# Kernel optimization log

Measured on AMD Instinct MI355X. Metric: run time of the kernel, lower is better.

## Reference

```python
import jax, jax.numpy as jnp
import numpy as np

B, N, F = 1024, 256, 8
E = 1024
OUT = 128          # NNConv out-channels (hardcoded in module)
N_DIV = 64         # len(num_actions)
PER = 3            # actions per diverter
FEAT = N * OUT     # feature_size() = num_nodes * 128


def setup_inputs() -> dict:
    key = jax.random.key(0)
    ks = jax.random.split(key, 20)
    s = lambda *sh: 0.02
    return {
        "x": jax.random.normal(ks[0], (B, N, F), jnp.float32),
        "edge_index": jax.random.randint(ks[1], (2, E), 0, N, jnp.int64),
        # edge-MLP nn1: Linear(1,64) -> ReLU -> Linear(64, F*OUT)
        "w1": jax.random.normal(ks[2], (1, 64), jnp.float32) * 0.1,
        "b1": jnp.zeros((64,), jnp.float32),
        "w2": jax.random.normal(ks[3], (64, F * OUT), jnp.float32) * 0.02,
        "b2": jnp.zeros((F * OUT,), jnp.float32),
        # NNConv root weight + bias
        "root_w": jax.random.normal(ks[4], (F, OUT), jnp.float32) * 0.1,
        "conv_b": jnp.zeros((OUT,), jnp.float32),
        # dueling heads
        "adv_w": jax.random.normal(ks[5], (FEAT, N_DIV * PER), jnp.float32) * 0.005,
        "adv_b": jnp.zeros((N_DIV * PER,), jnp.float32),
        "v1w": jax.random.normal(ks[6], (FEAT, 64), jnp.float32) * 0.005,
        "v1b": jnp.zeros((64,), jnp.float32),
        "v2w": jax.random.normal(ks[7], (64, 64), jnp.float32) * 0.1,
        "v2b": jnp.zeros((64,), jnp.float32),
        "v3w": jax.random.normal(ks[8], (64, N_DIV), jnp.float32) * 0.1,
        "v3b": jnp.zeros((N_DIV,), jnp.float32),
    }


def reference(x, edge_index, w1, b1, w2, b2, root_w, conv_b,
              adv_w, adv_b, v1w, v1b, v2w, v2b, v3w, v3b):
    b, n, f = x.shape
    out_c = root_w.shape[1]
    n_div = v3w.shape[1]
    flat = x.reshape(b * n, f)                              # [B*N, F]
    e = edge_index.shape[1]
    # edge_attr = ones -> edge MLP produces per-edge weight matrix theta
    ea = jnp.ones((e, 1), x.dtype)
    h = jax.nn.relu(ea @ w1 + b1)
    theta = (h @ w2 + b2).reshape(e, f, out_c)              # [E, F, OUT]
    src, tgt = edge_index[0], edge_index[1]
    # gather source feats -> per-edge matmul -> scatter-add at targets
    msg = jnp.einsum('ef,efo->eo', flat[src], theta)        # [E, OUT]
    agg = jnp.zeros((b * n, out_c), x.dtype).at[tgt].add(msg)
    conv = agg + flat @ root_w + conv_b                      # NNConv root + bias
    feat = jax.nn.relu(conv).reshape(b, -1)                  # [B, N*OUT]
    adv = jax.nn.relu(feat @ adv_w + adv_b).reshape(b, n_div, -1)
    val = jax.nn.relu(feat @ v1w + v1b)
    val = jax.nn.relu(val @ v2w + v2b)
    val = val @ v3w + v3b                                    # [B, n_div]
    return val[..., None] + adv - adv.mean(-1, keepdims=True)
```

## Files before the change

### kernel.cpp

```cpp
#include <hip/hip_runtime.h>

#define Bsz 1024
#define Nn 256
#define Fdim 8
#define Eedge 1024
#define OUTC 128
#define CADV 192
#define CTOT 256
#define Ktot 32768
#define ASTR 40
#define XSTR 24

typedef __attribute__((ext_vector_type(8))) short short8;
typedef __attribute__((ext_vector_type(4))) float float4v;

static __device__ inline unsigned short f2bf(float f) {
  union { float f; unsigned u; } v; v.f = f;
  unsigned r = v.u + 0x7FFFu + ((v.u >> 16) & 1u);
  return (unsigned short)(r >> 16);
}
static __device__ inline float bf2f(unsigned short h) {
  union { unsigned u; float f; } v; v.u = ((unsigned)h) << 16;
  return v.f;
}
static __device__ inline uint4 pack8(const unsigned short* b) {
  uint4 v;
  v.x = (unsigned)b[0] | ((unsigned)b[1] << 16);
  v.y = (unsigned)b[2] | ((unsigned)b[3] << 16);
  v.z = (unsigned)b[4] | ((unsigned)b[5] << 16);
  v.w = (unsigned)b[6] | ((unsigned)b[7] << 16);
  return v;
}
static __device__ inline unsigned cvtpk(float a, float b) {
  unsigned r;
  asm("v_cvt_pk_bf16_f32 %0, %1, %2" : "=v"(r) : "v"(a), "v"(b));
  return r;
}
static __device__ inline float hi_of(unsigned p)  {
  union { unsigned u; float f; } v; v.u = p << 16; return v.f;
}
static __device__ inline float hi2_of(unsigned p) {
  union { unsigned u; float f; } v; v.u = p & 0xFFFF0000u; return v.f;
}

__global__ __launch_bounds__(256) void prep_feat_kernel(
    const float* __restrict__ x, const int* __restrict__ ei,
    const float* __restrict__ w1, const float* __restrict__ b1,
    const float* __restrict__ w2, const float* __restrict__ b2,
    const float* __restrict__ rootw, const float* __restrict__ convb,
    const float* __restrict__ advw, const float* __restrict__ v1w,
    unsigned short* __restrict__ wt, unsigned short* __restrict__ feat0)
{
  __shared__ __align__(16) char smem[20480];
  int bid = blockIdx.x, t = threadIdx.x;

  if (bid < 16) {
    float* fs   = (float*)smem;
    float* h_s  = fs;
    float* rw_s = fs + 64;
    float* th_s = fs + 128;
    float* pt_s = fs + 192;
    float* S_s  = fs + 448;
    int*   flag = (int*)(fs + 2496);
    int obase = bid * 8;

    if (t < 64) {
      h_s[t]  = fmaxf(w1[t] + b1[t], 0.f);
      rw_s[t] = rootw[(t >> 3) * OUTC + obase + (t & 7)];
    }
    for (int i = t; i < Nn * Fdim; i += 256) S_s[i] = 0.f;
    if (t == 0) {
      int z = 0;
      for (int i = 1; i < 16; i += 2) z |= ei[i];
      *flag = (z == 0);
    }
    __syncthreads();
    int is64 = *flag;

    {
      int l = t & 63, g = t >> 6;
      int c = (l >> 3) * 128 + obase + (l & 7);
      float p = 0.f;
#pragma unroll
      for (int j = 0; j < 16; ++j)
        p += h_s[g * 16 + j] * w2[(size_t)(g * 16 + j) * 1024 + c];
      pt_s[t] = p;
    }
    int srcs[4], tgts[4];
#pragma unroll
    for (int q = 0; q < 4; ++q) {
      int e = t + q * 256;
      if (is64) { srcs[q] = ei[2 * e]; tgts[q] = ei[2 * (Eedge + e)]; }
      else      { srcs[q] = ei[e];     tgts[q] = ei[Eedge + e]; }
      srcs[q] &= 255; tgts[q] &= 255;
    }
    __syncthreads();
    if (t < 64) {
      int c = (t >> 3) * 128 + obase + (t & 7);
      th_s[t] = b2[c] + pt_s[t] + pt_s[t + 64] + pt_s[t + 128] + pt_s[t + 192];
    }
#pragma unroll
    for (int q = 0; q < 4; ++q) {
      const float* xp = x + srcs[q] * Fdim;
#pragma unroll
      for (int f = 0; f < Fdim; ++f)
        atomicAdd(&S_s[tgts[q] * Fdim + f], xp[f]);
    }
    __syncthreads();
    {
      int n = t;
      const float* xp = x + n * Fdim;
      float4 xa = *(const float4*)xp;
      float4 xb = *(const float4*)(xp + 4);
      float xv[8] = {xa.x, xa.y, xa.z, xa.w, xb.x, xb.y, xb.z, xb.w};
      float sv[8];
#pragma unroll
      for (int f = 0; f < 8; ++f) sv[f] = S_s[n * Fdim + f];
      unsigned short buf[8];
#pragma unroll
      for (int oi = 0; oi < 8; ++oi) {
        float z = convb[obase + oi];
#pragma unroll
        for (int f = 0; f < 8; ++f)
          z += xv[f] * rw_s[f * 8 + oi] + sv[f] * th_s[f * 8 + oi];
        buf[oi] = f2bf(fmaxf(z, 0.f));
      }
      *(uint4*)(feat0 + (size_t)n * OUTC + obase) = pack8(buf);
    }
  } else {
    unsigned short* st = (unsigned short*)smem;
    int kt = bid - 16, c = t;
    const float* src; int stride, col;
    if (c < CADV) { src = advw; stride = CADV; col = c; }
    else          { src = v1w;  stride = 64;   col = c - CADV; }
    float v[32];
#pragma unroll
    for (int i = 0; i < 32; ++i)
      v[i] = src[(size_t)(kt * 32 + i) * stride + col];
    unsigned pk[16];
#pragma unroll
    for (int i = 0; i < 16; ++i) pk[i] = cvtpk(v[2 * i], v[2 * i + 1]);
#pragma unroll
    for (int p = 0; p < 4; ++p) {
      uint4 w4; w4.x = pk[p * 4]; w4.y = pk[p * 4 + 1];
      w4.z = pk[p * 4 + 2]; w4.w = pk[p * 4 + 3];
      *(uint4*)(st + c * ASTR + p * 8) = w4;
    }
    __syncthreads();
    uint4* dst = (uint4*)(wt + (size_t)kt * (CTOT * 32));
    for (int r = 0; r < 4; ++r) {
      int s = r * 256 + c;
      dst[s] = *(const uint4*)(st + (s >> 2) * ASTR + (s & 3) * 8);
    }
  }
}

__global__ __launch_bounds__(512, 2) void gemm_mfma(
    const float* __restrict__ x, const unsigned short* __restrict__ wt,
    const float* __restrict__ rootw, const float* __restrict__ convb,
    const unsigned short* __restrict__ feat0, float* __restrict__ part,
    int iters, int ns)
{
  __shared__ short a_s[2][128 * ASTR];
  __shared__ short b_s[2][256 * ASTR];
  __shared__ short x_s[2][128 * XSTR];
  __shared__ short rw_s[128 * XSTR];
  __shared__ float convb_s[128];
  int t = threadIdx.x;
  int ch = blockIdx.x;
  int mb = blockIdx.y;
  int wave = t >> 6, lane = t & 63;
  int wm = wave >> 2, wn = wave & 3;
  int lm = lane & 15, lq = lane >> 4;

  float4v acc[4][4];
#pragma unroll
  for (int i = 0; i < 4; ++i)
#pragma unroll
    for (int j = 0; j < 4; ++j) acc[i][j] = (float4v)0.f;

  int kt0 = ch * iters;
  int iters4 = iters >> 2;
  int n0 = ch * iters4;
  int wr0 = (t >> 2) * ASTR + (t & 3) * 8;
  int u1 = t + 512;
  int wr1 = (u1 >> 2) * ASTR + (u1 & 3) * 8;

  if (t < 128) {
    float wv[8];
#pragma unroll
    for (int f = 0; f < 8; ++f) wv[f] = rootw[f * OUTC + t];
    unsigned ph[4];
#pragma unroll
    for (int i = 0; i < 4; ++i) ph[i] = cvtpk(wv[2 * i], wv[2 * i + 1]);
    float wl[8];
#pragma unroll
    for (int i = 0; i < 4; ++i) {
      wl[2 * i]     = wv[2 * i]     - hi_of(ph[i]);
      wl[2 * i + 1] = wv[2 * i + 1] - hi2_of(ph[i]);
    }
    unsigned pl[4];
#pragma unroll
    for (int i = 0; i < 4; ++i) pl[i] = cvtpk(wl[2 * i], wl[2 * i + 1]);
    uint4 wh4; wh4.x = ph[0]; wh4.y = ph[1]; wh4.z = ph[2]; wh4.w = ph[3];
    uint4 wl4; wl4.x = pl[0]; wl4.y = pl[1]; wl4.z = pl[2]; wl4.w = pl[3];
    *(uint4*)(rw_s + t * XSTR)     = wh4;
    *(uint4*)(rw_s + t * XSTR + 8) = wl4;
    convb_s[t] = convb[t];
  }
  int xr = (t & 255) >> 1, xh = t & 1;
  const float* xgb = x + ((size_t)(mb * 128 + xr) * Nn) * Fdim + xh * 4;
  if (t < 256) {
    float4 xv = *(const float4*)(xgb + (size_t)n0 * Fdim);
    uint2 dh, dl;
    dh.x = cvtpk(xv.x, xv.y);
    dh.y = cvtpk(xv.z, xv.w);
    dl.x = cvtpk(xv.x - hi_of(dh.x), xv.y - hi2_of(dh.x));
    dl.y = cvtpk(xv.z - hi_of(dh.y), xv.w - hi2_of(dh.y));
    *(uint2*)(x_s[0] + xr * XSTR + xh * 4)     = dh;
    *(uint2*)(x_s[0] + xr * XSTR + 8 + xh * 4) = dl;
  }
  __syncthreads();

  {
    int bloc = wave * 16 + lm;
    short8 xf = (short8)0;
    if (lq == 0 || lq == 2) xf = *(const short8*)(x_s[0] + bloc * XSTR);
    else if (lq == 1)       xf = *(const short8*)(x_s[0] + bloc * XSTR + 8);
#pragma unroll
    for (int tt = 0; tt < 2; ++tt) {
      int ot = tt;
      short8 wf = (short8)0;
      if (lq <= 1)      wf = *(const short8*)(rw_s + (ot * 16 + lm) * XSTR);
      else if (lq == 2) wf = *(const short8*)(rw_s + (ot * 16 + lm) * XSTR + 8);
      float4v c = __builtin_amdgcn_mfma_f32_16x16x32_bf16(wf, xf, (float4v)0.f, 0, 0, 0);
      int o0 = ot * 16 + lq * 4;
      float4 cb = *(const float4*)(convb_s + o0);
      unsigned d0 = cvtpk(fmaxf(c[0] + cb.x, 0.f), fmaxf(c[1] + cb.y, 0.f));
      unsigned d1 = cvtpk(fmaxf(c[2] + cb.z, 0.f), fmaxf(c[3] + cb.w, 0.f));
      if (mb == 0 && bloc == 0) {
        const unsigned* f0p = (const unsigned*)(feat0 + ((size_t)n0 * OUTC + o0));
        d0 = f0p[0]; d1 = f0p[1];
      }
      uint2 dd; dd.x = d0; dd.y = d1;
      *(uint2*)(a_s[0] + bloc * ASTR + tt * 16 + lq * 4) = dd;
    }
  }

  const uint4* gB = (const uint4*)wt + (size_t)kt0 * 1024;
  uint4 vb0 = gB[t], vb1 = gB[t + 512];
  float4 xpf = {0.f, 0.f, 0.f, 0.f};

  for (int kk = 0; kk < iters; ++kk) {
    int g = kk & 3, grp = kk >> 2;
    short* bb = b_s[kk & 1];
    *(uint4*)(bb + wr0) = vb0;
    *(uint4*)(bb + wr1) = vb1;
    if (g == 0 && grp + 1 < iters4 && t < 256)
      xpf = *(const float4*)(xgb + (size_t)(n0 + grp + 1) * Fdim);
    if (g == 3 && grp + 1 < iters4 && t < 256) {
      uint2 dh, dl;
      dh.x = cvtpk(xpf.x, xpf.y);
      dh.y = cvtpk(xpf.z, xpf.w);
      dl.x = cvtpk(xpf.x - hi_of(dh.x), xpf.y - hi2_of(dh.x));
      dl.y = cvtpk(xpf.z - hi_of(dh.y), xpf.w - hi2_of(dh.y));
      short* xd = x_s[(grp + 1) & 1];
      *(uint2*)(xd + xr * XSTR + xh * 4)     = dh;
      *(uint2*)(xd + xr * XSTR + 8 + xh * 4) = dl;
    }
    if (kk + 1 < iters) {
      const uint4* gB2 = (const uint4*)wt + (size_t)(kt0 + kk + 1) * 1024;
      vb0 = gB2[t]; vb1 = gB2[t + 512];
    }
    __syncthreads();

    short* ab = a_s[kk & 1];
    short8 aF[4];
#pragma unroll
    for (int i = 0; i < 4; ++i)
      aF[i] = *(const short8*)(ab + (wm * 64 + i * 16 + lm) * ASTR + lq * 8);
#pragma unroll
    for (int j = 0; j < 4; ++j) {
      short8 bF = *(const short8*)(bb + (wn * 64 + j * 16 + lm) * ASTR + lq * 8);
#pragma unroll
      for (int i = 0; i < 4; ++i)
        acc[i][j] = __builtin_amdgcn_mfma_f32_16x16x32_bf16(bF, aF[i], acc[i][j], 0, 0, 0);
    }

    if (kk + 1 < iters) {
      int kn = kk + 1;
      int g2 = kn & 3, grp2 = kn >> 2;
      const short* xs = x_s[grp2 & 1];
      int node2 = n0 + grp2;
      short* ad = a_s[kn & 1];
      int bloc = wave * 16 + lm;
      short8 xf = (short8)0;
      if (lq == 0 || lq == 2) xf = *(const short8*)(xs + bloc * XSTR);
      else if (lq == 1)       xf = *(const short8*)(xs + bloc * XSTR + 8);
#pragma unroll
      for (int tt = 0; tt < 2; ++tt) {
        int ot = g2 * 2 + tt;
        short8 wf = (short8)0;
        if (lq <= 1)      wf = *(const short8*)(rw_s + (ot * 16 + lm) * XSTR);
        else if (lq == 2) wf = *(const short8*)(rw_s + (ot * 16 + lm) * XSTR + 8);
        float4v c = __builtin_amdgcn_mfma_f32_16x16x32_bf16(wf, xf, (float4v)0.f, 0, 0, 0);
        int o0 = ot * 16 + lq * 4;
        float4 cb = *(const float4*)(convb_s + o0);
        unsigned d0 = cvtpk(fmaxf(c[0] + cb.x, 0.f), fmaxf(c[1] + cb.y, 0.f));
        unsigned d1 = cvtpk(fmaxf(c[2] + cb.z, 0.f), fmaxf(c[3] + cb.w, 0.f));
        if (mb == 0 && bloc == 0) {
          const unsigned* f0p = (const unsigned*)(feat0 + ((size_t)node2 * OUTC + o0));
          d0 = f0p[0]; d1 = f0p[1];
        }
        uint2 dd; dd.x = d0; dd.y = d1;
        *(uint2*)(ad + bloc * ASTR + tt * 16 + lq * 4) = dd;
      }
    }
  }

  float* pb = part + ((size_t)(mb * 128) * ns + ch) * CTOT;
#pragma unroll
  for (int i = 0; i < 4; ++i) {
    int m = wm * 64 + i * 16 + lm;
#pragma unroll
    for (int j = 0; j < 4; ++j) {
      int c = wn * 64 + j * 16 + lq * 4;
      *(float4v*)(pb + (size_t)m * ns * CTOT + c) = acc[i][j];
    }
  }
}

__global__ __launch_bounds__(256) void final_kernel(
    const float* __restrict__ part, int ns,
    const float* __restrict__ advb, const float* __restrict__ v1b,
    const float* __restrict__ v2w, const float* __restrict__ v2b,
    const float* __restrict__ v3w, const float* __restrict__ v3b,
    float* __restrict__ out)
{
  __shared__ float4v red_s[4][64];
  __shared__ float adv_s[CADV];
  __shared__ float v1_s[64];
  __shared__ float val2_s[64];
  __shared__ float val3_s[64];
  int b = blockIdx.x, t = threadIdx.x;
  int q = t & 63, r0 = t >> 6;
  const float4v* p4 = (const float4v*)(part + (size_t)b * ns * CTOT);
  float4v s4 = (float4v)0.f;
  for (int i = r0; i < ns; i += 4) s4 += p4[i * 64 + q];
  red_s[r0][q] = s4;
  __syncthreads();
  float s;
  {
    const float* rs = (const float*)red_s;
    s = rs[t] + rs[256 + t] + rs[512 + t] + rs[768 + t];
  }
  if (t < CADV) adv_s[t] = fmaxf(s + advb[t], 0.f);
  else          v1_s[t - CADV] = fmaxf(s + v1b[t - CADV], 0.f);
  __syncthreads();
  if (t < 64) {
    float a = v2b[t];
#pragma unroll
    for (int i = 0; i < 64; ++i) a += v1_s[i] * v2w[i * 64 + t];
    val2_s[t] = fmaxf(a, 0.f);
  }
  __syncthreads();
  if (t < 64) {
    float a = v3b[t];
#pragma unroll
    for (int j = 0; j < 64; ++j) a += val2_s[j] * v3w[j * 64 + t];
    val3_s[t] = a;
  }
  __syncthreads();
  if (t < CADV) {
    int d = t / 3;
    float mean = (adv_s[d * 3] + adv_s[d * 3 + 1] + adv_s[d * 3 + 2]) * (1.f / 3.f);
    out[(size_t)b * CADV + t] = val3_s[d] + adv_s[t] - mean;
  }
}

extern "C" void kernel_launch(void* const* d_in, const int* in_sizes, int n_in,
                              void* d_out, int out_size, void* d_ws, size_t ws_size,
                              hipStream_t stream)
{
  (void)in_sizes; (void)n_in; (void)out_size;
  const float* x     = (const float*)d_in[0];
  const int*   ei    = (const int*)d_in[1];
  const float* w1    = (const float*)d_in[2];
  const float* b1    = (const float*)d_in[3];
  const float* w2    = (const float*)d_in[4];
  const float* b2    = (const float*)d_in[5];
  const float* rootw = (const float*)d_in[6];
  const float* convb = (const float*)d_in[7];
  const float* advw  = (const float*)d_in[8];
  const float* advb  = (const float*)d_in[9];
  const float* v1w   = (const float*)d_in[10];
  const float* v1b   = (const float*)d_in[11];
  const float* v2w   = (const float*)d_in[12];
  const float* v2b   = (const float*)d_in[13];
  const float* v3w   = (const float*)d_in[14];
  const float* v3b   = (const float*)d_in[15];
  float* out = (float*)d_out;

  const size_t f0B = 131072;
  const size_t wtB = (size_t)Ktot * CTOT * 2;

  int NS = 64;
  while (NS > 8 && f0B + wtB + (size_t)NS * Bsz * CTOT * 4 > ws_size)
    NS >>= 1;

  unsigned short* feat0 = (unsigned short*)d_ws;
  unsigned short* wtp   = (unsigned short*)((char*)d_ws + f0B);
  float* part = (float*)((char*)d_ws + f0B + wtB);

  prep_feat_kernel<<<1040, 256, 0, stream>>>(x, ei, w1, b1, w2, b2, rootw,
                                             convb, advw, v1w, wtp, feat0);
  gemm_mfma<<<dim3(NS, 8), 512, 0, stream>>>(x, wtp, rootw, convb, feat0, part,
                                             1024 / NS, NS);
  final_kernel<<<Bsz, 256, 0, stream>>>(part, NS, advb, v1b, v2w, v2b, v3w, v3b, out);
}
```

Before: 166.4 us.

## Halve GEMM M-tile to 64 rows and rebalance split-K with more batch blocks

The main GEMM block now covers 64 batch rows instead of 128, launching 16 M-blocks instead of 8, and the split-K count drops from 64 to 32 so each block runs twice as many K iterations. The on-the-fly A-tile generation (root conv, bias, ReLU) is spread so each wave computes one 16x16 output subtile. The aim is to halve the partial-sum buffer written and reduced by the final kernel and to lower per-block LDS and register use. In exchange the same B tiles (weights) are streamed by twice as many M-blocks, so each weight load is reused over fewer rows, and per-block work becomes longer.

Result: no change. 165.5 us (-0.5%).

```diff
diff --git a/kernel.cpp b/kernel.cpp
--- a/kernel.cpp
+++ b/kernel.cpp
@@ -161,9 +161,9 @@
     const unsigned short* __restrict__ feat0, float* __restrict__ part,
     int iters, int ns)
 {
-  __shared__ short a_s[2][128 * ASTR];
+  __shared__ short a_s[2][64 * ASTR];
   __shared__ short b_s[2][256 * ASTR];
-  __shared__ short x_s[2][128 * XSTR];
+  __shared__ short x_s[2][64 * XSTR];
   __shared__ short rw_s[128 * XSTR];
   __shared__ float convb_s[128];
   int t = threadIdx.x;
@@ -173,9 +173,9 @@
   int wm = wave >> 2, wn = wave & 3;
   int lm = lane & 15, lq = lane >> 4;
 
-  float4v acc[4][4];
-#pragma unroll
-  for (int i = 0; i < 4; ++i)
+  float4v acc[2][4];
+#pragma unroll
+  for (int i = 0; i < 2; ++i)
 #pragma unroll
     for (int j = 0; j < 4; ++j) acc[i][j] = (float4v)0.f;
 
@@ -185,6 +185,8 @@
   int wr0 = (t >> 2) * ASTR + (t & 3) * 8;
   int u1 = t + 512;
   int wr1 = (u1 >> 2) * ASTR + (u1 & 3) * 8;
+  int grow = (wave & 3) * 16 + lm;
+  int gtt  = wave >> 2;
 
   if (t < 128) {
     float wv[8];
@@ -208,9 +210,9 @@
     *(uint4*)(rw_s + t * XSTR + 8) = wl4;
     convb_s[t] = convb[t];
   }
-  int xr = (t & 255) >> 1, xh = t & 1;
-  const float* xgb = x + ((size_t)(mb * 128 + xr) * Nn) * Fdim + xh * 4;
-  if (t < 256) {
+  int xr = (t & 127) >> 1, xh = t & 1;
+  const float* xgb = x + ((size_t)(mb * 64 + xr) * Nn) * Fdim + xh * 4;
+  if (t < 128) {
     float4 xv = *(const float4*)(xgb + (size_t)n0 * Fdim);
     uint2 dh, dl;
     dh.x = cvtpk(xv.x, xv.y);
@@ -223,13 +225,76 @@
   __syncthreads();
 
   {
-    int bloc = wave * 16 + lm;
     short8 xf = (short8)0;
-    if (lq == 0 || lq == 2) xf = *(const short8*)(x_s[0] + bloc * XSTR);
-    else if (lq == 1)       xf = *(const short8*)(x_s[0] + bloc * XSTR + 8);
-#pragma unroll
-    for (int tt = 0; tt < 2; ++tt) {
-      int ot = tt;
+    if (lq == 0 || lq == 2) xf = *(const short8*)(x_s[0] + grow * XSTR);
+    else if (lq == 1)       xf = *(const short8*)(x_s[0] + grow * XSTR + 8);
+    int ot = gtt;
+    short8 wf = (short8)0;
+    if (lq <= 1)      wf = *(const short8*)(rw_s + (ot * 16 + lm) * XSTR);
+    else if (lq == 2) wf = *(const short8*)(rw_s + (ot * 16 + lm) * XSTR + 8);
+    float4v c = __builtin_amdgcn_mfma_f32_16x16x32_bf16(wf, xf, (float4v)0.f, 0, 0, 0);
+    int o0 = ot * 16 + lq * 4;
+    float4 cb = *(const float4*)(convb_s + o0);
+    unsigned d0 = cvtpk(fmaxf(c[0] + cb.x, 0.f), fmaxf(c[1] + cb.y, 0.f));
+    unsigned d1 = cvtpk(fmaxf(c[2] + cb.z, 0.f), fmaxf(c[3] + cb.w, 0.f));
+    if (mb == 0 && grow == 0) {
+      const unsigned* f0p = (const unsigned*)(feat0 + ((size_t)n0 * OUTC + o0));
+      d0 = f0p[0]; d1 = f0p[1];
+    }
+    uint2 dd; dd.x = d0; dd.y = d1;
+    *(uint2*)(a_s[0] + grow * ASTR + gtt * 16 + lq * 4) = dd;
+  }
+
+  const uint4* gB = (const uint4*)wt + (size_t)kt0 * 1024;
+  uint4 vb0 = gB[t], vb1 = gB[t + 512];
+  float4 xpf = {0.f, 0.f, 0.f, 0.f};
+
+  for (int kk = 0; kk < iters; ++kk) {
+    int g = kk & 3, grp = kk >> 2;
+    short* bb = b_s[kk & 1];
+    *(uint4*)(bb + wr0) = vb0;
+    *(uint4*)(bb + wr1) = vb1;
+    if (g == 0 && grp + 1 < iters4 && t < 128)
+      xpf = *(const float4*)(xgb + (size_t)(n0 + grp + 1) * Fdim);
+    if (g == 3 && grp + 1 < iters4 && t < 128) {
+      uint2 dh, dl;
+      dh.x = cvtpk(xpf.x, xpf.y);
+      dh.y = cvtpk(xpf.z, xpf.w);
+      dl.x = cvtpk(xpf.x - hi_of(dh.x), xpf.y - hi2_of(dh.x));
+      dl.y = cvtpk(xpf.z - hi_of(dh.y), xpf.w - hi2_of(dh.y));
+      short* xd = x_s[(grp + 1) & 1];
+      *(uint2*)(xd + xr * XSTR + xh * 4)     = dh;
+      *(uint2*)(xd + xr * XSTR + 8 + xh * 4) = dl;
+    }
+    if (kk + 1 < iters) {
+      const uint4* gB2 = (const uint4*)wt + (size_t)(kt0 + kk + 1) * 1024;
+      vb0 = gB2[t]; vb1 = gB2[t + 512];
+    }
+    __syncthreads();
+
+    short* ab = a_s[kk & 1];
+    short8 aF[2];
+#pragma unroll
+    for (int i = 0; i < 2; ++i)
+      aF[i] = *(const short8*)(ab + (wm * 32 + i * 16 + lm) * ASTR + lq * 8);
+#pragma unroll
+    for (int j = 0; j < 4; ++j) {
+      short8 bF = *(const short8*)(bb + (wn * 64 + j * 16 + lm) * ASTR + lq * 8);
+#pragma unroll
+      for (int i = 0; i < 2; ++i)
+        acc[i][j] = __builtin_amdgcn_mfma_f32_16x16x32_bf16(bF, aF[i], acc[i][j], 0, 0, 0);
+    }
+
+    if (kk + 1 < iters) {
+      int kn = kk + 1;
+      int g2 = kn & 3, grp2 = kn >> 2;
+      const short* xs = x_s[grp2 & 1];
+      int node2 = n0 + grp2;
+      short* ad = a_s[kn & 1];
+      short8 xf = (short8)0;
+      if (lq == 0 || lq == 2) xf = *(const short8*)(xs + grow * XSTR);
+      else if (lq == 1)       xf = *(const short8*)(xs + grow * XSTR + 8);
+      int ot = g2 * 2 + gtt;
       short8 wf = (short8)0;
       if (lq <= 1)      wf = *(const short8*)(rw_s + (ot * 16 + lm) * XSTR);
       else if (lq == 2) wf = *(const short8*)(rw_s + (ot * 16 + lm) * XSTR + 8);
@@ -238,90 +303,19 @@
       float4 cb = *(const float4*)(convb_s + o0);
       unsigned d0 = cvtpk(fmaxf(c[0] + cb.x, 0.f), fmaxf(c[1] + cb.y, 0.f));
       unsigned d1 = cvtpk(fmaxf(c[2] + cb.z, 0.f), fmaxf(c[3] + cb.w, 0.f));
-      if (mb == 0 && bloc == 0) {
-        const unsigned* f0p = (const unsigned*)(feat0 + ((size_t)n0 * OUTC + o0));
+      if (mb == 0 && grow == 0) {
+        const unsigned* f0p = (const unsigned*)(feat0 + ((size_t)node2 * OUTC + o0));
         d0 = f0p[0]; d1 = f0p[1];
       }
       uint2 dd; dd.x = d0; dd.y = d1;
-      *(uint2*)(a_s[0] + bloc * ASTR + tt * 16 + lq * 4) = dd;
-    }
-  }
-
-  const uint4* gB = (const uint4*)wt + (size_t)kt0 * 1024;
-  uint4 vb0 = gB[t], vb1 = gB[t + 512];
-  float4 xpf = {0.f, 0.f, 0.f, 0.f};
-
-  for (int kk = 0; kk < iters; ++kk) {
-    int g = kk & 3, grp = kk >> 2;
-    short* bb = b_s[kk & 1];
-    *(uint4*)(bb + wr0) = vb0;
-    *(uint4*)(bb + wr1) = vb1;
-    if (g == 0 && grp + 1 < iters4 && t < 256)
-      xpf = *(const float4*)(xgb + (size_t)(n0 + grp + 1) * Fdim);
-    if (g == 3 && grp + 1 < iters4 && t < 256) {
-      uint2 dh, dl;
-      dh.x = cvtpk(xpf.x, xpf.y);
-      dh.y = cvtpk(xpf.z, xpf.w);
-      dl.x = cvtpk(xpf.x - hi_of(dh.x), xpf.y - hi2_of(dh.x));
-      dl.y = cvtpk(xpf.z - hi_of(dh.y), xpf.w - hi2_of(dh.y));
-      short* xd = x_s[(grp + 1) & 1];
-      *(uint2*)(xd + xr * XSTR + xh * 4)     = dh;
-      *(uint2*)(xd + xr * XSTR + 8 + xh * 4) = dl;
-    }
-    if (kk + 1 < iters) {
-      const uint4* gB2 = (const uint4*)wt + (size_t)(kt0 + kk + 1) * 1024;
-      vb0 = gB2[t]; vb1 = gB2[t + 512];
-    }
-    __syncthreads();
-
-    short* ab = a_s[kk & 1];
-    short8 aF[4];
-#pragma unroll
-    for (int i = 0; i < 4; ++i)
-      aF[i] = *(const short8*)(ab + (wm * 64 + i * 16 + lm) * ASTR + lq * 8);
-#pragma unroll
-    for (int j = 0; j < 4; ++j) {
-      short8 bF = *(const short8*)(bb + (wn * 64 + j * 16 + lm) * ASTR + lq * 8);
-#pragma unroll
-      for (int i = 0; i < 4; ++i)
-        acc[i][j] = __builtin_amdgcn_mfma_f32_16x16x32_bf16(bF, aF[i], acc[i][j], 0, 0, 0);
-    }
-
-    if (kk + 1 < iters) {
-      int kn = kk + 1;
-      int g2 = kn & 3, grp2 = kn >> 2;
-      const short* xs = x_s[grp2 & 1];
-      int node2 = n0 + grp2;
-      short* ad = a_s[kn & 1];
-      int bloc = wave * 16 + lm;
-      short8 xf = (short8)0;
-      if (lq == 0 || lq == 2) xf = *(const short8*)(xs + bloc * XSTR);
-      else if (lq == 1)       xf = *(const short8*)(xs + bloc * XSTR + 8);
-#pragma unroll
-      for (int tt = 0; tt < 2; ++tt) {
-        int ot = g2 * 2 + tt;
-        short8 wf = (short8)0;
-        if (lq <= 1)      wf = *(const short8*)(rw_s + (ot * 16 + lm) * XSTR);
-        else if (lq == 2) wf = *(const short8*)(rw_s + (ot * 16 + lm) * XSTR + 8);
-        float4v c = __builtin_amdgcn_mfma_f32_16x16x32_bf16(wf, xf, (float4v)0.f, 0, 0, 0);
-        int o0 = ot * 16 + lq * 4;
-        float4 cb = *(const float4*)(convb_s + o0);
-        unsigned d0 = cvtpk(fmaxf(c[0] + cb.x, 0.f), fmaxf(c[1] + cb.y, 0.f));
-        unsigned d1 = cvtpk(fmaxf(c[2] + cb.z, 0.f), fmaxf(c[3] + cb.w, 0.f));
-        if (mb == 0 && bloc == 0) {
-          const unsigned* f0p = (const unsigned*)(feat0 + ((size_t)node2 * OUTC + o0));
-          d0 = f0p[0]; d1 = f0p[1];
-        }
-        uint2 dd; dd.x = d0; dd.y = d1;
-        *(uint2*)(ad + bloc * ASTR + tt * 16 + lq * 4) = dd;
-      }
-    }
-  }
-
-  float* pb = part + ((size_t)(mb * 128) * ns + ch) * CTOT;
-#pragma unroll
-  for (int i = 0; i < 4; ++i) {
-    int m = wm * 64 + i * 16 + lm;
+      *(uint2*)(ad + grow * ASTR + gtt * 16 + lq * 4) = dd;
+    }
+  }
+
+  float* pb = part + ((size_t)(mb * 64) * ns + ch) * CTOT;
+#pragma unroll
+  for (int i = 0; i < 2; ++i) {
+    int m = wm * 32 + i * 16 + lm;
 #pragma unroll
     for (int j = 0; j < 4; ++j) {
       int c = wn * 64 + j * 16 + lq * 4;
@@ -404,7 +398,7 @@
   const size_t f0B = 131072;
   const size_t wtB = (size_t)Ktot * CTOT * 2;
 
-  int NS = 64;
+  int NS = 32;
   while (NS > 8 && f0B + wtB + (size_t)NS * Bsz * CTOT * 4 > ws_size)
     NS >>= 1;
 
@@ -414,7 +408,7 @@
 
   prep_feat_kernel<<<1040, 256, 0, stream>>>(x, ei, w1, b1, w2, b2, rootw,
                                              convb, advw, v1w, wtp, feat0);
-  gemm_mfma<<<dim3(NS, 8), 512, 0, stream>>>(x, wtp, rootw, convb, feat0, part,
-                                             1024 / NS, NS);
+  gemm_mfma<<<dim3(NS, 16), 512, 0, stream>>>(x, wtp, rootw, convb, feat0, part,
+                                              1024 / NS, NS);
   final_kernel<<<Bsz, 256, 0, stream>>>(part, NS, advb, v1b, v2w, v2b, v3w, v3b, out);
 }
```
